# Kernel tuning notes

Measured on AMD Instinct MI355X. Metric: run time of the kernel, lower is better.

## Reference

```python
import jax, jax.numpy as jnp
import numpy as np

N = 1_000_000
IN_DIM = 256
HIDDEN = 32
NUM_SEG = 100_000


def setup_inputs() -> dict:
    key = jax.random.key(0)
    ks = jax.random.split(key, 6)
    review_x = jax.random.normal(ks[0], (N, IN_DIM), dtype=jnp.float32)
    Wq = jax.random.normal(ks[1], (IN_DIM, HIDDEN), dtype=jnp.float32) * (1.0 / np.sqrt(IN_DIM))
    bq = jax.random.normal(ks[2], (HIDDEN,), dtype=jnp.float32) * 0.01
    Wk = jax.random.normal(ks[3], (IN_DIM, HIDDEN), dtype=jnp.float32) * (1.0 / np.sqrt(IN_DIM))
    bk = jax.random.normal(ks[4], (HIDDEN,), dtype=jnp.float32) * 0.01
    review_to_rest_idx = jax.random.randint(ks[5], (N,), 0, NUM_SEG, dtype=jnp.int64 if jax.config.jax_enable_x64 else jnp.int32)
    return {
        "review_x": review_x,
        "Wq": Wq,
        "bq": bq,
        "Wk": Wk,
        "bk": bk,
        "review_to_rest_idx": review_to_rest_idx,
        "num_segments": NUM_SEG,
    }


def reference(review_x, Wq, bq, Wk, bk, review_to_rest_idx, num_segments):
    # q/k projections: [N, hidden]
    qv = review_x @ Wq + bq
    kv = review_x @ Wk + bk
    # attention logits per review: [N]
    att = jnp.sum(qv * kv, axis=-1)
    idx = review_to_rest_idx
    # segment softmax (numerically stable): max, exp, sum per restaurant group
    seg_max = jax.ops.segment_max(att, idx, num_segments=num_segments)
    # empty segments yield -inf max; never gathered, but keep finite for safety
    seg_max = jnp.where(jnp.isfinite(seg_max), seg_max, 0.0)
    e = jnp.exp(att - seg_max[idx])
    seg_sum = jax.ops.segment_sum(e, idx, num_segments=num_segments)
    weights = e / seg_sum[idx]
    return weights
```

## Files before the change

### kernel.cpp

```cpp
#include <hip/hip_runtime.h>
#include <hip/hip_fp16.h>
#include <math.h>

#define IN_DIM 256
#define HID 32
#define NSEG 100000

typedef _Float16 half8 __attribute__((ext_vector_type(8)));
typedef __fp16  fp16x2 __attribute__((ext_vector_type(2)));
typedef float floatx4 __attribute__((ext_vector_type(4)));

__global__ __launch_bounds__(256, 2) void att_kernel(
    const float* __restrict__ x,
    const float* __restrict__ Wq, const float* __restrict__ bq,
    const float* __restrict__ Wk, const float* __restrict__ bk,
    const int* __restrict__ idx,
    float* __restrict__ e_out, float* __restrict__ segsum,
    int n, int nsub)
{
    __shared__ _Float16 BF[4 * 8 * 64 * 8];

    const int tid = threadIdx.x;
    const int w  = tid >> 6, l = tid & 63;
    const int lr = l & 15,  lg = l >> 4;

    {
        const int ks = tid >> 5, lg2 = (tid >> 3) & 3, j = tid & 7;
        const float4* wqr = (const float4*)(Wq + (size_t)tid * HID);
        const float4* wkr = (const float4*)(Wk + (size_t)tid * HID);
#pragma unroll
        for (int i = 0; i < 8; ++i) {
            float4 vq = wqr[i];
            float4 vk = wkr[i];
            float fq[4] = { vq.x, vq.y, vq.z, vq.w };
            float fk[4] = { vk.x, vk.y, vk.z, vk.w };
#pragma unroll
            for (int u2 = 0; u2 < 4; ++u2) {
                int c = i * 4 + u2, cg = c >> 4, cr = c & 15;
                BF[(((cg    ) * 8 + ks) * 64 + lg2 * 16 + cr) * 8 + j] = (_Float16)fq[u2];
                BF[(((cg + 2) * 8 + ks) * 64 + lg2 * 16 + cr) * 8 + j] = (_Float16)fk[u2];
            }
        }
    }
    __syncthreads();
    half8 b[4][8];
    {
        const _Float16* bfl = BF + (size_t)l * 8;
#pragma unroll
        for (int cg = 0; cg < 4; ++cg)
#pragma unroll
            for (int ks = 0; ks < 8; ++ks)
                b[cg][ks] = *(const half8*)(bfl + (cg * 8 + ks) * 512);
    }

    const float bq0 = bq[lr], bq1 = bq[lr + 16];
    const float bk0 = bk[lr], bk1 = bk[lr + 16];

    const int gw      = blockIdx.x * 4 + w;
    const int gstride = gridDim.x * 4;

    int s = gw;
    if (s >= nsub) return;

    float4 raw[16];
    {
        int row = s * 16 + lr; if (row >= n) row = n - 1;
        const float* xp = x + (size_t)row * IN_DIM + lg * 8;
#pragma unroll
        for (int ks = 0; ks < 8; ++ks) {
            raw[2 * ks]     = *(const float4*)(xp + ks * 32);
            raw[2 * ks + 1] = *(const float4*)(xp + ks * 32 + 4);
        }
    }

    while (true) {
        const int snext = s + gstride;

        half8 a[8];
#pragma unroll
        for (int ks = 0; ks < 8; ++ks) {
            float4 v0 = raw[2 * ks], v1 = raw[2 * ks + 1];
            union { half8 h8; fp16x2 h2[4]; } u;
            u.h2[0] = __builtin_amdgcn_cvt_pkrtz(v0.x, v0.y);
            u.h2[1] = __builtin_amdgcn_cvt_pkrtz(v0.z, v0.w);
            u.h2[2] = __builtin_amdgcn_cvt_pkrtz(v1.x, v1.y);
            u.h2[3] = __builtin_amdgcn_cvt_pkrtz(v1.z, v1.w);
            a[ks] = u.h8;
        }

        if (snext < nsub) {
            int row = snext * 16 + lr; if (row >= n) row = n - 1;
            const float* xp = x + (size_t)row * IN_DIM + lg * 8;
#pragma unroll
            for (int ks = 0; ks < 8; ++ks) {
                raw[2 * ks]     = *(const float4*)(xp + ks * 32);
                raw[2 * ks + 1] = *(const float4*)(xp + ks * 32 + 4);
            }
        }
        __builtin_amdgcn_sched_barrier(0);

        floatx4 acc0 = {0.f,0.f,0.f,0.f}, acc1 = {0.f,0.f,0.f,0.f};
        floatx4 acc2 = {0.f,0.f,0.f,0.f}, acc3 = {0.f,0.f,0.f,0.f};
#pragma unroll
        for (int ks = 0; ks < 8; ++ks) {
            acc0 = __builtin_amdgcn_mfma_f32_16x16x32_f16(a[ks], b[0][ks], acc0, 0, 0, 0);
            acc1 = __builtin_amdgcn_mfma_f32_16x16x32_f16(a[ks], b[1][ks], acc1, 0, 0, 0);
            acc2 = __builtin_amdgcn_mfma_f32_16x16x32_f16(a[ks], b[2][ks], acc2, 0, 0, 0);
            acc3 = __builtin_amdgcn_mfma_f32_16x16x32_f16(a[ks], b[3][ks], acc3, 0, 0, 0);
        }

        float p[4];
#pragma unroll
        for (int i2 = 0; i2 < 4; ++i2) {
            p[i2] = (acc0[i2] + bq0) * (acc2[i2] + bk0)
                  + (acc1[i2] + bq1) * (acc3[i2] + bk1);
            p[i2] += __shfl_xor(p[i2], 1);
            p[i2] += __shfl_xor(p[i2], 2);
            p[i2] += __shfl_xor(p[i2], 4);
            p[i2] += __shfl_xor(p[i2], 8);
        }

        if (lr < 4) {
            float pv = (lr & 1) ? ((lr & 2) ? p[3] : p[1])
                                : ((lr & 2) ? p[2] : p[0]);
            int r = s * 16 + lg * 4 + lr;
            if (r < n) {
                float e = __expf(pv);
                e_out[r] = e;
                atomicAdd(&segsum[idx[r]], e);
            }
        }

        if (snext >= nsub) break;
        s = snext;
    }
}

__global__ __launch_bounds__(256) void norm_kernel(
    const int* __restrict__ idx, const float* __restrict__ segsum,
    float* __restrict__ out, int n)
{
    int i = blockIdx.x * blockDim.x + threadIdx.x;
    int stride = gridDim.x * blockDim.x;
    int n4 = n >> 2;
    for (; i < n4; i += stride) {
        float4 e = ((const float4*)out)[i];
        int4  s4 = ((const int4*)idx)[i];
        float4 r;
        r.x = e.x / segsum[s4.x];
        r.y = e.y / segsum[s4.y];
        r.z = e.z / segsum[s4.z];
        r.w = e.w / segsum[s4.w];
        ((float4*)out)[i] = r;
    }
    if (blockIdx.x == 0 && threadIdx.x < (n & 3)) {
        int j = (n & ~3) + threadIdx.x;
        out[j] = out[j] / segsum[idx[j]];
    }
}

extern "C" void kernel_launch(void* const* d_in, const int* in_sizes, int n_in,
                              void* d_out, int out_size, void* d_ws, size_t ws_size,
                              hipStream_t stream)
{
    const float* x   = (const float*)d_in[0];
    const float* Wq  = (const float*)d_in[1];
    const float* bq  = (const float*)d_in[2];
    const float* Wk  = (const float*)d_in[3];
    const float* bk  = (const float*)d_in[4];
    const int*   idx = (const int*)d_in[5];
    const int n = in_sizes[5];

    float* segsum = (float*)d_ws;

    (void)hipMemsetAsync(segsum, 0, (size_t)NSEG * 4, stream);

    const int nsub = (n + 15) >> 4;
    int grid1 = 512;
    if (grid1 * 4 > nsub) grid1 = (nsub + 3) / 4;
    att_kernel<<<grid1, 256, 0, stream>>>(x, Wq, bq, Wk, bk, idx,
                                          (float*)d_out, segsum, n, nsub);

    int n4 = n >> 2;
    int grid2 = (n4 + 255) / 256;
    if (grid2 > 1024) grid2 = 1024;
    if (grid2 < 1) grid2 = 1;
    norm_kernel<<<grid2, 256, 0, stream>>>(idx, segsum, (float*)d_out, n);
}
```

Before: 244.8 us.

## Read weight fragments from LDS per step to raise occupancy, prefetch segment index

The 32 half8 weight fragments are no longer held in registers; each iteration reloads them from shared memory right before the MFMAs. The freed registers let launch bounds rise from 2 to 3 blocks per SM and the grid grow from 512 to 768 blocks. The segment index for the next tile is now fetched together with the next x prefetch, which hides the idx load latency before the atomic. The cost is extra LDS traffic every iteration, plus a redundant reload of the current tile on the last iteration.

```diff
diff --git a/kernel.cpp b/kernel.cpp
--- a/kernel.cpp
+++ b/kernel.cpp
@@ -10,7 +10,7 @@
 typedef __fp16  fp16x2 __attribute__((ext_vector_type(2)));
 typedef float floatx4 __attribute__((ext_vector_type(4)));
 
-__global__ __launch_bounds__(256, 2) void att_kernel(
+__global__ __launch_bounds__(256, 3) void att_kernel(
     const float* __restrict__ x,
     const float* __restrict__ Wq, const float* __restrict__ bq,
     const float* __restrict__ Wk, const float* __restrict__ bk,
@@ -43,18 +43,11 @@
         }
     }
     __syncthreads();
-    half8 b[4][8];
-    {
-        const _Float16* bfl = BF + (size_t)l * 8;
-#pragma unroll
-        for (int cg = 0; cg < 4; ++cg)
-#pragma unroll
-            for (int ks = 0; ks < 8; ++ks)
-                b[cg][ks] = *(const half8*)(bfl + (cg * 8 + ks) * 512);
-    }
 
     const float bq0 = bq[lr], bq1 = bq[lr + 16];
     const float bk0 = bk[lr], bk1 = bk[lr + 16];
+
+    const _Float16* bfl = BF + (size_t)l * 8;
 
     const int gw      = blockIdx.x * 4 + w;
     const int gstride = gridDim.x * 4;
@@ -72,6 +65,8 @@
             raw[2 * ks + 1] = *(const float4*)(xp + ks * 32 + 4);
         }
     }
+    int r_ep = s * 16 + lg * 4 + lr;
+    int my_seg = idx[r_ep < n ? r_ep : (n - 1)];
 
     while (true) {
         const int snext = s + gstride;
@@ -87,15 +82,20 @@
             u.h2[3] = __builtin_amdgcn_cvt_pkrtz(v1.z, v1.w);
             a[ks] = u.h8;
         }
+        __builtin_amdgcn_sched_barrier(0);
 
-        if (snext < nsub) {
-            int row = snext * 16 + lr; if (row >= n) row = n - 1;
+        int r_next, seg_next;
+        {
+            int sc = snext < nsub ? snext : s;
+            int row = sc * 16 + lr; if (row >= n) row = n - 1;
             const float* xp = x + (size_t)row * IN_DIM + lg * 8;
 #pragma unroll
             for (int ks = 0; ks < 8; ++ks) {
                 raw[2 * ks]     = *(const float4*)(xp + ks * 32);
                 raw[2 * ks + 1] = *(const float4*)(xp + ks * 32 + 4);
             }
+            r_next = sc * 16 + lg * 4 + lr;
+            seg_next = idx[r_next < n ? r_next : (n - 1)];
         }
         __builtin_amdgcn_sched_barrier(0);
 
@@ -103,10 +103,14 @@
         floatx4 acc2 = {0.f,0.f,0.f,0.f}, acc3 = {0.f,0.f,0.f,0.f};
 #pragma unroll
         for (int ks = 0; ks < 8; ++ks) {
-            acc0 = __builtin_amdgcn_mfma_f32_16x16x32_f16(a[ks], b[0][ks], acc0, 0, 0, 0);
-            acc1 = __builtin_amdgcn_mfma_f32_16x16x32_f16(a[ks], b[1][ks], acc1, 0, 0, 0);
-            acc2 = __builtin_amdgcn_mfma_f32_16x16x32_f16(a[ks], b[2][ks], acc2, 0, 0, 0);
-            acc3 = __builtin_amdgcn_mfma_f32_16x16x32_f16(a[ks], b[3][ks], acc3, 0, 0, 0);
+            half8 b0 = *(const half8*)(bfl + (0 * 8 + ks) * 512);
+            half8 b1 = *(const half8*)(bfl + (1 * 8 + ks) * 512);
+            half8 b2 = *(const half8*)(bfl + (2 * 8 + ks) * 512);
+            half8 b3 = *(const half8*)(bfl + (3 * 8 + ks) * 512);
+            acc0 = __builtin_amdgcn_mfma_f32_16x16x32_f16(a[ks], b0, acc0, 0, 0, 0);
+            acc1 = __builtin_amdgcn_mfma_f32_16x16x32_f16(a[ks], b1, acc1, 0, 0, 0);
+            acc2 = __builtin_amdgcn_mfma_f32_16x16x32_f16(a[ks], b2, acc2, 0, 0, 0);
+            acc3 = __builtin_amdgcn_mfma_f32_16x16x32_f16(a[ks], b3, acc3, 0, 0, 0);
         }
 
         float p[4];
@@ -120,19 +124,18 @@
             p[i2] += __shfl_xor(p[i2], 8);
         }
 
-        if (lr < 4) {
+        if (lr < 4 && r_ep < n) {
             float pv = (lr & 1) ? ((lr & 2) ? p[3] : p[1])
                                 : ((lr & 2) ? p[2] : p[0]);
-            int r = s * 16 + lg * 4 + lr;
-            if (r < n) {
-                float e = __expf(pv);
-                e_out[r] = e;
-                atomicAdd(&segsum[idx[r]], e);
-            }
+            float e = __expf(pv);
+            e_out[r_ep] = e;
+            atomicAdd(&segsum[my_seg], e);
         }
 
         if (snext >= nsub) break;
         s = snext;
+        r_ep = r_next;
+        my_seg = seg_next;
     }
 }
 
@@ -176,7 +179,7 @@
     (void)hipMemsetAsync(segsum, 0, (size_t)NSEG * 4, stream);
 
     const int nsub = (n + 15) >> 4;
-    int grid1 = 512;
+    int grid1 = 768;
     if (grid1 * 4 > nsub) grid1 = (nsub + 3) / 4;
     att_kernel<<<grid1, 256, 0, stream>>>(x, Wq, bq, Wk, bk, idx,
                                           (float*)d_out, segsum, n, nsub);
```

Result: faster. 229.3 us (-6.3%).
